# Kernel optimization log

Measured on AMD Instinct MI355X. Metric: run time of the kernel, lower is better.

Reference implementation:

```python
import jax, jax.numpy as jnp
import numpy as np

RADII = [2, 4]
EPS = 1e-6


def _avg_pool_hw(t, k):
    # valid avg-pool with kernel k, stride 1 over the last two dims
    nd = t.ndim
    win = (1,) * (nd - 2) + (k, k)
    s = jax.lax.reduce_window(t, 0.0, jax.lax.add, win, (1,) * nd, 'VALID')
    return s / float(k * k)


def _patch_cca(x, y, r):
    B, C1, H, W = x.shape
    C2 = y.shape[1]
    k = 2 * r + 1
    pad = ((0, 0), (0, 0), (r, r), (r, r))
    xp = jnp.pad(x, pad, mode='reflect')  # (B,C1,Hp,Wp)
    yp = jnp.pad(y, pad, mode='reflect')  # (B,C2,Hp,Wp)

    # local second moments via outer products + avg pooling
    xx = _avg_pool_hw(xp[:, :, None] * xp[:, None], k)  # (B,C1,C1,H,W)
    yy = _avg_pool_hw(yp[:, :, None] * yp[:, None], k)  # (B,C2,C2,H,W)
    xy = _avg_pool_hw(xp[:, :, None] * yp[:, None], k)  # (B,C1,C2,H,W)
    xm = _avg_pool_hw(xp, k)  # (B,C1,H,W)
    ym = _avg_pool_hw(yp, k)  # (B,C2,H,W)

    cxx = xx - xm[:, :, None] * xm[:, None]
    cyy = yy - ym[:, :, None] * ym[:, None]
    cxy = xy - xm[:, :, None] * ym[:, None]

    # move matrix dims last: (B,H,W,Ci,Cj)
    cxx = jnp.transpose(cxx, (0, 3, 4, 1, 2)) + EPS * jnp.eye(C1, dtype=x.dtype)
    cyy = jnp.transpose(cyy, (0, 3, 4, 1, 2)) + EPS * jnp.eye(C2, dtype=x.dtype)
    cxy = jnp.transpose(cxy, (0, 3, 4, 1, 2))

    lx_inv = jnp.linalg.inv(jnp.linalg.cholesky(cxx))  # (B,H,W,C1,C1)
    ly_inv = jnp.linalg.inv(jnp.linalg.cholesky(cyy))  # (B,H,W,C2,C2)
    corr = jnp.einsum('bhwij,bhwjk,bhwkl->bhwil', lx_inv, cxy, ly_inv)
    diag = jnp.diagonal(corr, axis1=-2, axis2=-1)  # (B,H,W,min(C1,C2))
    sim = jnp.abs(diag).sum(-1) / min(C1, C2)  # (B,H,W)
    return sim[:, None]  # (B,1,H,W)


def setup_inputs() -> dict:
    key = jax.random.key(0)
    kx, ky = jax.random.split(key)
    B, C, H, W = 2, 6, 512, 512
    x = jax.random.normal(kx, (B, C, H, W), dtype=jnp.float32)
    y = jax.random.normal(ky, (B, C, H, W), dtype=jnp.float32)
    return {'x': x, 'y': y}


def reference(x, y):
    # stack per-radius CCA maps on a trailing axis -> (B,1,H,W,len(RADII))
    return jnp.stack([_patch_cca(x, y, r) for r in RADII], axis=-1)
```

## Files before the change

kernel.cpp:

```cpp
#include <hip/hip_runtime.h>
#include <math.h>

typedef float v2f __attribute__((ext_vector_type(2)));
typedef float v4f __attribute__((ext_vector_type(4)));

#define LT(i,j) ((i)*((i)+1)/2 + (j))

__device__ __forceinline__ int reflect512(int i) {
  int a = (i < 0) ? -i : i;
  int b = 1022 - a;
  return (a < b) ? a : b;
}

constexpr int HB  = 520;
constexpr int PS  = 12;
constexpr int RS  = HB * PS;

__global__ __launch_bounds__(256)
void prep_interleave4(const float* __restrict__ xg, const float* __restrict__ yg,
                      float* __restrict__ zb) {
  constexpr int H = 512, W = 512, HW = H * W;
  constexpr int WQ = HB / 4;
  const int idx = blockIdx.x * 256 + threadIdx.x;
  if (idx >= 2 * HB * WQ) return;
  const int b  = idx / (HB * WQ);
  const int r2 = idx - b * (HB * WQ);
  const int hr = r2 / WQ;
  const int q  = r2 - hr * WQ;
  const int h  = reflect512(hr - 4);
  const int w0 = q * 4 - 4;
  const size_t rowbase = (size_t)b * 6 * HW + (size_t)h * W;

  float xv[6][4], yv[6][4];
  if (w0 >= 0 && w0 + 3 < W) {
    #pragma unroll
    for (int c = 0; c < 6; ++c) {
      const v4f vx = *(const v4f*)(xg + rowbase + (size_t)c * HW + w0);
      const v4f vy = *(const v4f*)(yg + rowbase + (size_t)c * HW + w0);
      #pragma unroll
      for (int j = 0; j < 4; ++j) { xv[c][j] = vx[j]; yv[c][j] = vy[j]; }
    }
  } else {
    #pragma unroll
    for (int j = 0; j < 4; ++j) {
      const int w = reflect512(w0 + j);
      #pragma unroll
      for (int c = 0; c < 6; ++c) {
        xv[c][j] = xg[rowbase + (size_t)c * HW + w];
        yv[c][j] = yg[rowbase + (size_t)c * HW + w];
      }
    }
  }

  float* o = zb + ((size_t)(b * HB + hr) * HB + q * 4) * PS;
  #pragma unroll
  for (int j = 0; j < 4; ++j) {
    v4f p0 = {xv[0][j], xv[1][j], xv[2][j], xv[3][j]};
    v4f p1 = {xv[4][j], xv[5][j], yv[0][j], yv[1][j]};
    v4f p2 = {yv[2][j], yv[3][j], yv[4][j], yv[5][j]};
    *(v4f*)(o + j * PS + 0) = p0;
    *(v4f*)(o + j * PS + 4) = p1;
    *(v4f*)(o + j * PS + 8) = p2;
  }
}

__device__ __forceinline__ float gget(const v2f* accd, const v2f* accs,
                                      int a, int b) {
  const int t = LT(a >> 1, b >> 1);
  if (((a & 1) == 0) && ((b & 1) == 0)) return accd[t].x;
  if (((a & 1) == 1) && ((b & 1) == 1)) return accd[t].y;
  if ((a & 1) == 0) return accs[t].x;
  return accs[t].y;
}

__device__ __forceinline__ void cholinv6(float* a) {
  #pragma unroll
  for (int j = 0; j < 6; ++j) {
    float d = a[LT(j,j)];
    #pragma unroll
    for (int p = 0; p < j; ++p) d -= a[LT(j,p)] * a[LT(j,p)];
    const float rd = __builtin_amdgcn_rsqf(d);
    a[LT(j,j)] = rd;
    #pragma unroll
    for (int i = j + 1; i < 6; ++i) {
      float s = a[LT(i,j)];
      #pragma unroll
      for (int p = 0; p < j; ++p) s -= a[LT(i,p)] * a[LT(j,p)];
      a[LT(i,j)] = s * rd;
    }
  }
  #pragma unroll
  for (int j = 0; j < 6; ++j) {
    #pragma unroll
    for (int i = j + 1; i < 6; ++i) {
      float s = 0.0f;
      #pragma unroll
      for (int p = j; p < i; ++p) s += a[LT(i,p)] * a[LT(p,j)];
      a[LT(i,j)] = -s * a[LT(i,i)];
    }
  }
}

template <int K, bool ADD>
__device__ __forceinline__ void row_acc_g(const float* __restrict__ p,
                                          v2f* zs, v2f* accd, v2f* accs) {
  #pragma unroll
  for (int dx = 0; dx < K; ++dx) {
    const v4f l0 = *(const v4f*)(p + dx * PS + 0);
    const v4f l1 = *(const v4f*)(p + dx * PS + 4);
    const v4f l2 = *(const v4f*)(p + dx * PS + 8);
    v2f z[6];
    z[0] = l0.lo; z[1] = l0.hi;
    z[2] = l1.lo; z[3] = l1.hi;
    z[4] = l2.lo; z[5] = l2.hi;
    #pragma unroll
    for (int q = 0; q < 6; ++q) zs[q] = ADD ? (zs[q] + z[q]) : (zs[q] - z[q]);
    int t = 0;
    #pragma unroll
    for (int Kp = 0; Kp < 6; ++Kp) {
      #pragma unroll
      for (int Pp = 0; Pp <= Kp; ++Pp) {
        const v2f c  = z[Pp];
        const v2f cs = __builtin_shufflevector(c, c, 1, 0);
        const v2f a  = ADD ? z[Kp] : -z[Kp];
        accd[t] = __builtin_elementwise_fma(a, c,  accd[t]);
        accs[t] = __builtin_elementwise_fma(a, cs, accs[t]);
        ++t;
      }
    }
  }
}

template <int K>
__device__ __forceinline__ float emit_sim(const v2f* zs, const v2f* accd,
                                          const v2f* accs) {
  constexpr float inv_n = 1.0f / (K * K);
  float mx[6], my[6];
  #pragma unroll
  for (int i = 0; i < 6; ++i) {
    mx[i] = ((i & 1) ? zs[i >> 1].y : zs[i >> 1].x) * inv_n;
    my[i] = ((i & 1) ? zs[3 + (i >> 1)].y : zs[3 + (i >> 1)].x) * inv_n;
  }
  float ax[21];
  {
    int t = 0;
    #pragma unroll
    for (int i = 0; i < 6; ++i)
      #pragma unroll
      for (int j = 0; j <= i; ++j) {
        const float e = (i == j) ? 1e-6f : 0.0f;
        ax[t] = gget(accd, accs, i, j) * inv_n - mx[i] * mx[j] + e;
        ++t;
      }
  }
  cholinv6(ax);
  float ay[21];
  {
    int t = 0;
    #pragma unroll
    for (int i = 0; i < 6; ++i)
      #pragma unroll
      for (int j = 0; j <= i; ++j) {
        const float e = (i == j) ? 1e-6f : 0.0f;
        ay[t] = gget(accd, accs, 6 + i, 6 + j) * inv_n - my[i] * my[j] + e;
        ++t;
      }
  }
  cholinv6(ay);
  float cxy[36];
  #pragma unroll
  for (int i = 0; i < 6; ++i)
    #pragma unroll
    for (int j = 0; j < 6; ++j)
      cxy[i * 6 + j] = fmaf(-mx[i], my[j], gget(accd, accs, 6 + j, i) * inv_n);
  float sim = 0.0f;
  #pragma unroll
  for (int i = 0; i < 6; ++i) {
    float di = 0.0f;
    #pragma unroll
    for (int j = 0; j <= i; ++j) {
      float inner = 0.0f;
      #pragma unroll
      for (int k = i; k < 6; ++k) inner += cxy[j * 6 + k] * ay[LT(k, i)];
      di += ax[LT(i, j)] * inner;
    }
    sim += fabsf(di);
  }
  return sim * (1.0f / 6.0f);
}

template <int R, int V>
__device__ __forceinline__ void run(const float* __restrict__ zb,
                                    float* __restrict__ out, int b, int ri,
                                    int h0) {
  constexpr int K = 2 * R + 1;
  constexpr int H = 512, W = 512;

  const int w0 = blockIdx.x * 16;
  const int tx = threadIdx.x & 15;
  const int g  = threadIdx.x >> 4;
  const int hbase = h0 + g * V;
  const int wc = w0 + tx;

  const float* base = zb + (size_t)b * HB * RS
                    + (size_t)(hbase + 4 - R) * RS + (size_t)(wc + 4 - R) * PS;

  v2f zs[6]    = {};
  v2f accd[21] = {};
  v2f accs[21] = {};

  #pragma unroll 1
  for (int dy = 0; dy < K; ++dy)
    row_acc_g<K, true>(base + dy * RS, zs, accd, accs);

  out[((size_t)((b * H + hbase) * W + wc)) * 2 + ri] =
      emit_sim<K>(zs, accd, accs);

  #pragma unroll 1
  for (int s = 1; s < V; ++s) {
    row_acc_g<K, true >(base + (s + 2 * R) * RS, zs, accd, accs);
    row_acc_g<K, false>(base + (s - 1)     * RS, zs, accd, accs);
    out[((size_t)((b * H + hbase + s) * W + wc)) * 2 + ri] =
        emit_sim<K>(zs, accd, accs);
  }
}

__global__ __launch_bounds__(256, 2)
void cca_bal(const float* __restrict__ zb, float* __restrict__ out) {
  const int z = blockIdx.z;
  if (z < 2) {
    run<4, 4>(zb, out, z, 1, (int)blockIdx.y * (16 * 4));
  } else {
    const int b = (int)(blockIdx.y >> 2);
    run<2, 8>(zb, out, b, 0, (int)(blockIdx.y & 3) * (16 * 8));
  }
}

extern "C" void kernel_launch(void* const* d_in, const int* in_sizes, int n_in,
                              void* d_out, int out_size, void* d_ws, size_t ws_size,
                              hipStream_t stream) {
  const float* x = (const float*)d_in[0];
  const float* y = (const float*)d_in[1];
  float* out = (float*)d_out;
  float* zb  = (float*)d_ws;

  {
    const int n = 2 * HB * (HB / 4);
    prep_interleave4<<<dim3((n + 255) / 256), dim3(256), 0, stream>>>(x, y, zb);
  }
  dim3 grid(512 / 16, 8, 3);
  cca_bal<<<grid, dim3(256), 0, stream>>>(zb, out);
}
```

Baseline: 151.5 us.

## Accumulate per-column vertical windows and reduce horizontally with DPP lane shifts

Each thread now accumulates only one column of the K-tall window: for each row step it adds and subtracts a single pixel's outer products instead of K pixels. The horizontal K-wide sums of means and second moments are formed at emit time with DPP row_shr adds across neighbouring lanes in a 16-lane row. This cuts the per-output accumulation FMAs roughly by a factor of K. The costs are about 90 DPP reductions per output and halo lanes (2R of 16) that run the full Cholesky emit but discard the result. The grid is reorganised so radius-4 blocks produce 8 valid columns and radius-2 blocks produce 12, both with 8 rows per thread group.

Result: slower. 321.6 us (+112.3%).

```diff
diff --git a/kernel.cpp b/kernel.cpp
--- a/kernel.cpp
+++ b/kernel.cpp
@@ -73,6 +73,34 @@
   return accs[t].y;
 }
 
+template <int CTRL>
+__device__ __forceinline__ float dppadd(float dsrc, float acc) {
+  int d = __builtin_amdgcn_update_dpp(0, __float_as_int(dsrc), CTRL, 0xF, 0xF, true);
+  return acc + __int_as_float(d);
+}
+
+template <int K>
+__device__ __forceinline__ float redK(float x) {
+  if constexpr (K == 9) {
+    float s = dppadd<0x111>(x, x);
+    s = dppadd<0x112>(s, s);
+    s = dppadd<0x114>(s, s);
+    s = dppadd<0x118>(x, s);
+    return s;
+  } else {
+    float s = dppadd<0x111>(x, x);
+    s = dppadd<0x112>(s, s);
+    s = dppadd<0x114>(x, s);
+    return s;
+  }
+}
+
+template <int K>
+__device__ __forceinline__ float gget_r(const v2f* accd, const v2f* accs,
+                                        int a, int b) {
+  return redK<K>(gget(accd, accs, a, b));
+}
+
 __device__ __forceinline__ void cholinv6(float* a) {
   #pragma unroll
   for (int j = 0; j < 6; ++j) {
@@ -101,47 +129,57 @@
   }
 }
 
-template <int K, bool ADD>
-__device__ __forceinline__ void row_acc_g(const float* __restrict__ p,
-                                          v2f* zs, v2f* accd, v2f* accs) {
-  #pragma unroll
-  for (int dx = 0; dx < K; ++dx) {
-    const v4f l0 = *(const v4f*)(p + dx * PS + 0);
-    const v4f l1 = *(const v4f*)(p + dx * PS + 4);
-    const v4f l2 = *(const v4f*)(p + dx * PS + 8);
-    v2f z[6];
-    z[0] = l0.lo; z[1] = l0.hi;
-    z[2] = l1.lo; z[3] = l1.hi;
-    z[4] = l2.lo; z[5] = l2.hi;
-    #pragma unroll
-    for (int q = 0; q < 6; ++q) zs[q] = ADD ? (zs[q] + z[q]) : (zs[q] - z[q]);
+template <bool ADD>
+__device__ __forceinline__ void px_acc(const float* __restrict__ p,
+                                       v2f* zs, v2f* accd, v2f* accs) {
+  const v4f l0 = *(const v4f*)(p + 0);
+  const v4f l1 = *(const v4f*)(p + 4);
+  const v4f l2 = *(const v4f*)(p + 8);
+  v2f z[6];
+  z[0] = l0.lo; z[1] = l0.hi;
+  z[2] = l1.lo; z[3] = l1.hi;
+  z[4] = l2.lo; z[5] = l2.hi;
+  #pragma unroll
+  for (int q = 0; q < 6; ++q) zs[q] = ADD ? (zs[q] + z[q]) : (zs[q] - z[q]);
+  int t = 0;
+  #pragma unroll
+  for (int Kp = 0; Kp < 6; ++Kp) {
+    #pragma unroll
+    for (int Pp = 0; Pp <= Kp; ++Pp) {
+      const v2f c  = z[Pp];
+      const v2f cs = __builtin_shufflevector(c, c, 1, 0);
+      const v2f a  = ADD ? z[Kp] : -z[Kp];
+      accd[t] = __builtin_elementwise_fma(a, c,  accd[t]);
+      accs[t] = __builtin_elementwise_fma(a, cs, accs[t]);
+      ++t;
+    }
+  }
+}
+
+template <int K>
+__device__ __forceinline__ float emit_sim_dpp(const v2f* zs, const v2f* accd,
+                                              const v2f* accs) {
+  constexpr float inv_n = 1.0f / (K * K);
+  float mx[6], my[6];
+  #pragma unroll
+  for (int i = 0; i < 6; ++i) {
+    mx[i] = redK<K>((i & 1) ? zs[i >> 1].y : zs[i >> 1].x) * inv_n;
+    my[i] = redK<K>((i & 1) ? zs[3 + (i >> 1)].y : zs[3 + (i >> 1)].x) * inv_n;
+  }
+  float ax[21];
+  {
     int t = 0;
     #pragma unroll
-    for (int Kp = 0; Kp < 6; ++Kp) {
-      #pragma unroll
-      for (int Pp = 0; Pp <= Kp; ++Pp) {
-        const v2f c  = z[Pp];
-        const v2f cs = __builtin_shufflevector(c, c, 1, 0);
-        const v2f a  = ADD ? z[Kp] : -z[Kp];
-        accd[t] = __builtin_elementwise_fma(a, c,  accd[t]);
-        accs[t] = __builtin_elementwise_fma(a, cs, accs[t]);
+    for (int i = 0; i < 6; ++i)
+      #pragma unroll
+      for (int j = 0; j <= i; ++j) {
+        const float e = (i == j) ? 1e-6f : 0.0f;
+        ax[t] = gget_r<K>(accd, accs, i, j) * inv_n - mx[i] * mx[j] + e;
         ++t;
       }
-    }
-  }
-}
-
-template <int K>
-__device__ __forceinline__ float emit_sim(const v2f* zs, const v2f* accd,
-                                          const v2f* accs) {
-  constexpr float inv_n = 1.0f / (K * K);
-  float mx[6], my[6];
-  #pragma unroll
-  for (int i = 0; i < 6; ++i) {
-    mx[i] = ((i & 1) ? zs[i >> 1].y : zs[i >> 1].x) * inv_n;
-    my[i] = ((i & 1) ? zs[3 + (i >> 1)].y : zs[3 + (i >> 1)].x) * inv_n;
-  }
-  float ax[21];
+  }
+  cholinv6(ax);
+  float ay[21];
   {
     int t = 0;
     #pragma unroll
@@ -149,30 +187,17 @@
       #pragma unroll
       for (int j = 0; j <= i; ++j) {
         const float e = (i == j) ? 1e-6f : 0.0f;
-        ax[t] = gget(accd, accs, i, j) * inv_n - mx[i] * mx[j] + e;
+        ay[t] = gget_r<K>(accd, accs, 6 + i, 6 + j) * inv_n - my[i] * my[j] + e;
         ++t;
       }
   }
-  cholinv6(ax);
-  float ay[21];
-  {
-    int t = 0;
-    #pragma unroll
-    for (int i = 0; i < 6; ++i)
-      #pragma unroll
-      for (int j = 0; j <= i; ++j) {
-        const float e = (i == j) ? 1e-6f : 0.0f;
-        ay[t] = gget(accd, accs, 6 + i, 6 + j) * inv_n - my[i] * my[j] + e;
-        ++t;
-      }
-  }
   cholinv6(ay);
   float cxy[36];
   #pragma unroll
   for (int i = 0; i < 6; ++i)
     #pragma unroll
     for (int j = 0; j < 6; ++j)
-      cxy[i * 6 + j] = fmaf(-mx[i], my[j], gget(accd, accs, 6 + j, i) * inv_n);
+      cxy[i * 6 + j] = fmaf(-mx[i], my[j], gget_r<K>(accd, accs, 6 + j, i) * inv_n);
   float sim = 0.0f;
   #pragma unroll
   for (int i = 0; i < 6; ++i) {
@@ -190,49 +215,60 @@
 }
 
 template <int R, int V>
-__device__ __forceinline__ void run(const float* __restrict__ zb,
-                                    float* __restrict__ out, int b, int ri,
-                                    int h0) {
+__device__ __forceinline__ void run_dpp(const float* __restrict__ zb,
+                                        float* __restrict__ out, int b, int ri) {
   constexpr int K = 2 * R + 1;
   constexpr int H = 512, W = 512;
 
-  const int w0 = blockIdx.x * 16;
-  const int tx = threadIdx.x & 15;
-  const int g  = threadIdx.x >> 4;
-  const int hbase = h0 + g * V;
-  const int wc = w0 + tx;
-
-  const float* base = zb + (size_t)b * HB * RS
-                    + (size_t)(hbase + 4 - R) * RS + (size_t)(wc + 4 - R) * PS;
+  const int t  = threadIdx.x & 15;
+  const int G  = threadIdx.x >> 4;
+  const int gx0 = blockIdx.x * (16 - 2 * R);
+  const int hbase = ((int)blockIdx.y * 16 + G) * V;
+
+  int hc = gx0 + t + (4 - R);
+  if (hc > HB - 1) hc = HB - 1;
+  const float* colbase = zb + (size_t)b * HB * RS + (size_t)hc * PS;
 
   v2f zs[6]    = {};
   v2f accd[21] = {};
   v2f accs[21] = {};
 
+  const float* pw = colbase + (size_t)(hbase + 4 - R) * RS;
   #pragma unroll 1
-  for (int dy = 0; dy < K; ++dy)
-    row_acc_g<K, true>(base + dy * RS, zs, accd, accs);
-
-  out[((size_t)((b * H + hbase) * W + wc)) * 2 + ri] =
-      emit_sim<K>(zs, accd, accs);
-
+  for (int dy = 0; dy < K; ++dy) {
+    px_acc<true>(pw, zs, accd, accs);
+    pw += RS;
+  }
+
+  const int c0 = gx0 + t - 2 * R;
+  const bool valid = (t >= 2 * R) && (c0 < W);
+
+  {
+    const float sim = emit_sim_dpp<K>(zs, accd, accs);
+    if (valid)
+      out[((size_t)((b * H + hbase) * W + c0)) * 2 + ri] = sim;
+  }
+
+  const float* pe = colbase + (size_t)(hbase + 5 + R) * RS;
+  const float* pl = colbase + (size_t)(hbase + 4 - R) * RS;
   #pragma unroll 1
   for (int s = 1; s < V; ++s) {
-    row_acc_g<K, true >(base + (s + 2 * R) * RS, zs, accd, accs);
-    row_acc_g<K, false>(base + (s - 1)     * RS, zs, accd, accs);
-    out[((size_t)((b * H + hbase + s) * W + wc)) * 2 + ri] =
-        emit_sim<K>(zs, accd, accs);
+    px_acc<true >(pe, zs, accd, accs); pe += RS;
+    px_acc<false>(pl, zs, accd, accs); pl += RS;
+    const float sim = emit_sim_dpp<K>(zs, accd, accs);
+    if (valid)
+      out[((size_t)((b * H + hbase + s) * W + c0)) * 2 + ri] = sim;
   }
 }
 
 __global__ __launch_bounds__(256, 2)
-void cca_bal(const float* __restrict__ zb, float* __restrict__ out) {
+void cca_dpp(const float* __restrict__ zb, float* __restrict__ out) {
   const int z = blockIdx.z;
   if (z < 2) {
-    run<4, 4>(zb, out, z, 1, (int)blockIdx.y * (16 * 4));
+    run_dpp<4, 8>(zb, out, z, 1);
   } else {
-    const int b = (int)(blockIdx.y >> 2);
-    run<2, 8>(zb, out, b, 0, (int)(blockIdx.y & 3) * (16 * 8));
+    if (blockIdx.x >= 43) return;
+    run_dpp<2, 8>(zb, out, z - 2, 0);
   }
 }
 
@@ -248,6 +284,6 @@
     const int n = 2 * HB * (HB / 4);
     prep_interleave4<<<dim3((n + 255) / 256), dim3(256), 0, stream>>>(x, y, zb);
   }
-  dim3 grid(512 / 16, 8, 3);
-  cca_bal<<<grid, dim3(256), 0, stream>>>(zb, out);
-}
+  dim3 grid(64, 4, 4);
+  cca_dpp<<<grid, dim3(256), 0, stream>>>(zb, out);
+}
```

## Software-pipeline covariance extraction with Cholesky solve and rebalance radius grid

Applied to the files above, without the earlier changes.

Splits the per-pixel emit into extraction of the covariance matrices and a separate Cholesky-inverse and similarity step. The loop now overlaps the next row's sliding-window accumulation with finishing the previous pixel, which gives the scheduler independent work to interleave. The grid is also reshaped so both radii use 8 rows per thread across 4 z-slices, instead of 4 rows for radius 4 and 8 for radius 2. This raises register pressure, since 78 extra floats stay live across the accumulation, and risks spills at 2 blocks per CU. It also changes load balance, because radius-4 blocks now do more work each and there are fewer of them.

Measured after the change: 134.3 us. 11.4% less time.

```diff
diff --git a/kernel.cpp b/kernel.cpp
--- a/kernel.cpp
+++ b/kernel.cpp
@@ -132,8 +132,9 @@
 }
 
 template <int K>
-__device__ __forceinline__ float emit_sim(const v2f* zs, const v2f* accd,
-                                          const v2f* accs) {
+__device__ __forceinline__ void extract_emit(const v2f* zs, const v2f* accd,
+                                             const v2f* accs,
+                                             float* ax, float* ay, float* cxy) {
   constexpr float inv_n = 1.0f / (K * K);
   float mx[6], my[6];
   #pragma unroll
@@ -141,7 +142,6 @@
     mx[i] = ((i & 1) ? zs[i >> 1].y : zs[i >> 1].x) * inv_n;
     my[i] = ((i & 1) ? zs[3 + (i >> 1)].y : zs[3 + (i >> 1)].x) * inv_n;
   }
-  float ax[21];
   {
     int t = 0;
     #pragma unroll
@@ -150,29 +150,21 @@
       for (int j = 0; j <= i; ++j) {
         const float e = (i == j) ? 1e-6f : 0.0f;
         ax[t] = gget(accd, accs, i, j) * inv_n - mx[i] * mx[j] + e;
-        ++t;
-      }
-  }
-  cholinv6(ax);
-  float ay[21];
-  {
-    int t = 0;
-    #pragma unroll
-    for (int i = 0; i < 6; ++i)
-      #pragma unroll
-      for (int j = 0; j <= i; ++j) {
-        const float e = (i == j) ? 1e-6f : 0.0f;
         ay[t] = gget(accd, accs, 6 + i, 6 + j) * inv_n - my[i] * my[j] + e;
         ++t;
       }
   }
-  cholinv6(ay);
-  float cxy[36];
   #pragma unroll
   for (int i = 0; i < 6; ++i)
     #pragma unroll
     for (int j = 0; j < 6; ++j)
       cxy[i * 6 + j] = fmaf(-mx[i], my[j], gget(accd, accs, 6 + j, i) * inv_n);
+}
+
+__device__ __forceinline__ float finish_sim(float* ax, float* ay,
+                                            const float* cxy) {
+  cholinv6(ax);
+  cholinv6(ay);
   float sim = 0.0f;
   #pragma unroll
   for (int i = 0; i < 6; ++i) {
@@ -191,11 +183,11 @@
 
 template <int R, int V>
 __device__ __forceinline__ void run(const float* __restrict__ zb,
-                                    float* __restrict__ out, int b, int ri,
-                                    int h0) {
+                                    float* __restrict__ out, int b, int ri) {
   constexpr int K = 2 * R + 1;
   constexpr int H = 512, W = 512;
 
+  const int h0 = blockIdx.y * (16 * V);
   const int w0 = blockIdx.x * 16;
   const int tx = threadIdx.x & 15;
   const int g  = threadIdx.x >> 4;
@@ -213,27 +205,26 @@
   for (int dy = 0; dy < K; ++dy)
     row_acc_g<K, true>(base + dy * RS, zs, accd, accs);
 
-  out[((size_t)((b * H + hbase) * W + wc)) * 2 + ri] =
-      emit_sim<K>(zs, accd, accs);
+  float ax[21], ay[21], cxy[36];
+  extract_emit<K>(zs, accd, accs, ax, ay, cxy);
 
   #pragma unroll 1
   for (int s = 1; s < V; ++s) {
     row_acc_g<K, true >(base + (s + 2 * R) * RS, zs, accd, accs);
     row_acc_g<K, false>(base + (s - 1)     * RS, zs, accd, accs);
-    out[((size_t)((b * H + hbase + s) * W + wc)) * 2 + ri] =
-        emit_sim<K>(zs, accd, accs);
-  }
+    out[((size_t)((b * H + hbase + s - 1) * W + wc)) * 2 + ri] =
+        finish_sim(ax, ay, cxy);
+    extract_emit<K>(zs, accd, accs, ax, ay, cxy);
+  }
+  out[((size_t)((b * H + hbase + V - 1) * W + wc)) * 2 + ri] =
+      finish_sim(ax, ay, cxy);
 }
 
 __global__ __launch_bounds__(256, 2)
-void cca_bal(const float* __restrict__ zb, float* __restrict__ out) {
+void cca_pipe(const float* __restrict__ zb, float* __restrict__ out) {
   const int z = blockIdx.z;
-  if (z < 2) {
-    run<4, 4>(zb, out, z, 1, (int)blockIdx.y * (16 * 4));
-  } else {
-    const int b = (int)(blockIdx.y >> 2);
-    run<2, 8>(zb, out, b, 0, (int)(blockIdx.y & 3) * (16 * 8));
-  }
+  if (z < 2) run<2, 8>(zb, out, z, 0);
+  else       run<4, 8>(zb, out, z - 2, 1);
 }
 
 extern "C" void kernel_launch(void* const* d_in, const int* in_sizes, int n_in,
@@ -248,6 +239,6 @@
     const int n = 2 * HB * (HB / 4);
     prep_interleave4<<<dim3((n + 255) / 256), dim3(256), 0, stream>>>(x, y, zb);
   }
-  dim3 grid(512 / 16, 8, 3);
-  cca_bal<<<grid, dim3(256), 0, stream>>>(zb, out);
-}
+  dim3 grid(512 / 16, 512 / (16 * 8), 4);
+  cca_pipe<<<grid, dim3(256), 0, stream>>>(zb, out);
+}
```

## Stage incoming box-filter rows through double-buffered LDS with prefetch

Applied to the files above, without the earlier changes.

The main CCA kernel now loads each newly entering row of every thread's vertical segment cooperatively into a double-buffered LDS tile, prefetching the next row into registers while the current one is accumulated. Outgoing rows are still read from global memory. The grid is also rebalanced: both radii now use 8 rows per thread, with 4 z-slices instead of the previous uneven mix (R=4 with V=4). This is meant to cut redundant global/L2 traffic for the horizontal window and hide load latency. In exchange it adds a block-wide sync per row step and about 36KB of LDS per block, which may limit occupancy.

Result: faster. 141.3 us (-6.7%).

```diff
diff --git a/kernel.cpp b/kernel.cpp
--- a/kernel.cpp
+++ b/kernel.cpp
@@ -101,34 +101,38 @@
   }
 }
 
+template <bool ADD>
+__device__ __forceinline__ void px_acc(const float* __restrict__ p,
+                                       v2f* zs, v2f* accd, v2f* accs) {
+  const v4f l0 = *(const v4f*)(p + 0);
+  const v4f l1 = *(const v4f*)(p + 4);
+  const v4f l2 = *(const v4f*)(p + 8);
+  v2f z[6];
+  z[0] = l0.lo; z[1] = l0.hi;
+  z[2] = l1.lo; z[3] = l1.hi;
+  z[4] = l2.lo; z[5] = l2.hi;
+  #pragma unroll
+  for (int q = 0; q < 6; ++q) zs[q] = ADD ? (zs[q] + z[q]) : (zs[q] - z[q]);
+  int t = 0;
+  #pragma unroll
+  for (int Kp = 0; Kp < 6; ++Kp) {
+    #pragma unroll
+    for (int Pp = 0; Pp <= Kp; ++Pp) {
+      const v2f c  = z[Pp];
+      const v2f cs = __builtin_shufflevector(c, c, 1, 0);
+      const v2f a  = ADD ? z[Kp] : -z[Kp];
+      accd[t] = __builtin_elementwise_fma(a, c,  accd[t]);
+      accs[t] = __builtin_elementwise_fma(a, cs, accs[t]);
+      ++t;
+    }
+  }
+}
+
 template <int K, bool ADD>
 __device__ __forceinline__ void row_acc_g(const float* __restrict__ p,
                                           v2f* zs, v2f* accd, v2f* accs) {
   #pragma unroll
-  for (int dx = 0; dx < K; ++dx) {
-    const v4f l0 = *(const v4f*)(p + dx * PS + 0);
-    const v4f l1 = *(const v4f*)(p + dx * PS + 4);
-    const v4f l2 = *(const v4f*)(p + dx * PS + 8);
-    v2f z[6];
-    z[0] = l0.lo; z[1] = l0.hi;
-    z[2] = l1.lo; z[3] = l1.hi;
-    z[4] = l2.lo; z[5] = l2.hi;
-    #pragma unroll
-    for (int q = 0; q < 6; ++q) zs[q] = ADD ? (zs[q] + z[q]) : (zs[q] - z[q]);
-    int t = 0;
-    #pragma unroll
-    for (int Kp = 0; Kp < 6; ++Kp) {
-      #pragma unroll
-      for (int Pp = 0; Pp <= Kp; ++Pp) {
-        const v2f c  = z[Pp];
-        const v2f cs = __builtin_shufflevector(c, c, 1, 0);
-        const v2f a  = ADD ? z[Kp] : -z[Kp];
-        accd[t] = __builtin_elementwise_fma(a, c,  accd[t]);
-        accs[t] = __builtin_elementwise_fma(a, cs, accs[t]);
-        ++t;
-      }
-    }
-  }
+  for (int dx = 0; dx < K; ++dx) px_acc<ADD>(p + dx * PS, zs, accd, accs);
 }
 
 template <int K>
@@ -190,50 +194,95 @@
 }
 
 template <int R, int V>
-__device__ __forceinline__ void run(const float* __restrict__ zb,
-                                    float* __restrict__ out, int b, int ri,
-                                    int h0) {
-  constexpr int K = 2 * R + 1;
+__device__ __forceinline__ void run_lds(const float* __restrict__ zb,
+                                        float* __restrict__ out, int b, int ri,
+                                        float* __restrict__ lds) {
+  constexpr int K    = 2 * R + 1;
   constexpr int H = 512, W = 512;
-
+  constexpr int SEGW = 16 + 2 * R;
+  constexpr int CH   = SEGW * 3;
+  constexpr int NCH  = 16 * CH;
+  constexpr int NI   = (NCH + 255) / 256;
+  constexpr int SEGS = 288;
+  constexpr int BUFW = 16 * SEGS;
+  constexpr int PH   = K + V - 1;
+  constexpr int RSB  = RS * 4;
+
+  const int tid = threadIdx.x;
+  const int tx = tid & 15;
+  const int g  = tid >> 4;
+  const int h0 = blockIdx.y * (16 * V);
   const int w0 = blockIdx.x * 16;
-  const int tx = threadIdx.x & 15;
-  const int g  = threadIdx.x >> 4;
   const int hbase = h0 + g * V;
   const int wc = w0 + tx;
 
-  const float* base = zb + (size_t)b * HB * RS
-                    + (size_t)(hbase + 4 - R) * RS + (size_t)(wc + 4 - R) * PS;
+  int  goff[NI];
+  int  loff[NI];
+  bool act[NI];
+  #pragma unroll
+  for (int i = 0; i < NI; ++i) {
+    int q = tid + 256 * i;
+    act[i] = (q < NCH);
+    if (!act[i]) q = 0;
+    const int sg = q / CH;
+    const int of = q - sg * CH;
+    goff[i] = ((h0 + V * sg + 4 - R) * RS + (w0 + 4 - R) * PS + of * 4) * 4;
+    loff[i] = sg * SEGS + of * 4;
+  }
+  const char* zbB = (const char*)(zb + (size_t)b * HB * RS);
+  const float* lbase = zb + (size_t)b * HB * RS
+                     + (size_t)(hbase + 4 - R) * RS + (size_t)(wc + 4 - R) * PS;
+
+  #pragma unroll
+  for (int i = 0; i < NI; ++i) {
+    if (act[i]) {
+      const v4f v = *(const v4f*)(zbB + goff[i]);
+      *(v4f*)(lds + loff[i]) = v;
+    }
+  }
+  __syncthreads();
 
   v2f zs[6]    = {};
   v2f accd[21] = {};
   v2f accs[21] = {};
 
   #pragma unroll 1
-  for (int dy = 0; dy < K; ++dy)
-    row_acc_g<K, true>(base + dy * RS, zs, accd, accs);
-
-  out[((size_t)((b * H + hbase) * W + wc)) * 2 + ri] =
-      emit_sim<K>(zs, accd, accs);
-
-  #pragma unroll 1
-  for (int s = 1; s < V; ++s) {
-    row_acc_g<K, true >(base + (s + 2 * R) * RS, zs, accd, accs);
-    row_acc_g<K, false>(base + (s - 1)     * RS, zs, accd, accs);
-    out[((size_t)((b * H + hbase + s) * W + wc)) * 2 + ri] =
-        emit_sim<K>(zs, accd, accs);
+  for (int t = 0; t < PH; ++t) {
+    v4f st[NI];
+    const bool more = (t + 1 < PH);
+    if (more) {
+      #pragma unroll
+      for (int i = 0; i < NI; ++i)
+        if (act[i]) st[i] = *(const v4f*)(zbB + goff[i] + (t + 1) * RSB);
+    }
+    {
+      const float* ep = lds + (t & 1) * BUFW + g * SEGS + tx * 12;
+      #pragma unroll
+      for (int dx = 0; dx < K; ++dx)
+        px_acc<true>(ep + dx * 12, zs, accd, accs);
+    }
+    if (t >= K)
+      row_acc_g<K, false>(lbase + (size_t)(t - K) * RS, zs, accd, accs);
+    if (t >= K - 1) {
+      const float sim = emit_sim<K>(zs, accd, accs);
+      out[((size_t)((b * H + hbase + (t - K + 1)) * W + wc)) * 2 + ri] = sim;
+    }
+    if (more) {
+      float* wp = lds + ((t + 1) & 1) * BUFW;
+      #pragma unroll
+      for (int i = 0; i < NI; ++i)
+        if (act[i]) *(v4f*)(wp + loff[i]) = st[i];
+    }
+    __syncthreads();
   }
 }
 
 __global__ __launch_bounds__(256, 2)
-void cca_bal(const float* __restrict__ zb, float* __restrict__ out) {
+void cca_stage(const float* __restrict__ zb, float* __restrict__ out) {
+  __shared__ float lds[2][16][288];
   const int z = blockIdx.z;
-  if (z < 2) {
-    run<4, 4>(zb, out, z, 1, (int)blockIdx.y * (16 * 4));
-  } else {
-    const int b = (int)(blockIdx.y >> 2);
-    run<2, 8>(zb, out, b, 0, (int)(blockIdx.y & 3) * (16 * 8));
-  }
+  if (z < 2) run_lds<2, 8>(zb, out, z, 0, &lds[0][0][0]);
+  else       run_lds<4, 8>(zb, out, z - 2, 1, &lds[0][0][0]);
 }
 
 extern "C" void kernel_launch(void* const* d_in, const int* in_sizes, int n_in,
@@ -248,6 +297,6 @@
     const int n = 2 * HB * (HB / 4);
     prep_interleave4<<<dim3((n + 255) / 256), dim3(256), 0, stream>>>(x, y, zb);
   }
-  dim3 grid(512 / 16, 8, 3);
-  cca_bal<<<grid, dim3(256), 0, stream>>>(zb, out);
-}
+  dim3 grid(512 / 16, 512 / (16 * 8), 4);
+  cca_stage<<<grid, dim3(256), 0, stream>>>(zb, out);
+}
```
